# Optimization experiments

Hardware: AMD Instinct MI355X
Metric: run time of the kernel (lower is better)

## Reference

```python
import jax, jax.numpy as jnp
import numpy as np
import math

B = 64
N = 2048
EMBED_DIM = 128
N_HEADS = 8
VAL_DIM = EMBED_DIM // N_HEADS  # 16
KEY_DIM = VAL_DIM               # key_dim defaults to val_dim
CLIP = True
NORM = 1.0 / math.sqrt(KEY_DIM)


def _uniform_param(k, shape):
    # torch init: uniform(-stdv, stdv) with stdv = 1/sqrt(size(-1))
    stdv = 1.0 / math.sqrt(shape[-1])
    return jax.random.uniform(k, shape, jnp.float32, -stdv, stdv)


def setup_inputs() -> dict:
    key = jax.random.key(0)
    ks = jax.random.split(key, 11)
    h = jax.random.normal(ks[0], (B, N, EMBED_DIM), jnp.float32)
    adj_c = jax.random.randint(ks[1], (B, N, N), 0, 2).astype(jnp.float32)
    phone_set = jax.random.randint(ks[2], (B,), 1, N - 1)
    return dict(
        h=h, adj_c=adj_c, phone_set=phone_set,
        Wq_bf=_uniform_param(ks[3], (EMBED_DIM, KEY_DIM)),
        Wk_bf=_uniform_param(ks[4], (EMBED_DIM, KEY_DIM)),
        Wv_bf=_uniform_param(ks[5], (EMBED_DIM, VAL_DIM)),
        Wo_bf=_uniform_param(ks[6], (VAL_DIM, EMBED_DIM)),
        Wq_af=_uniform_param(ks[7], (EMBED_DIM, KEY_DIM)),
        Wk_af=_uniform_param(ks[8], (EMBED_DIM, KEY_DIM)),
        Wv_af=_uniform_param(ks[9], (EMBED_DIM, VAL_DIM)),
        Wo_af=_uniform_param(ks[10], (VAL_DIM, EMBED_DIM)),
    )


def _attend(h, h_phone, adj_row, pos_mask, Wq, Wk, Wv, Wo):
    # h: (B,N,D), h_phone: (B,D), adj_row: (B,N), pos_mask: (B,N) bool
    Q = h_phone @ Wq                              # (B,K)
    K = jnp.einsum('bnd,dk->bnk', h, Wk)          # (B,N,K)
    V = jnp.einsum('bnd,dk->bnk', h, Wv)          # (B,N,V)
    compat = NORM * jnp.einsum('bk,bnk->bn', Q, K)
    if CLIP:
        compat = 10.0 * jnp.tanh(compat)
    valid = pos_mask & (adj_row != 0)
    # masked stable softmax over valid positions; fully-masked rows -> zeros
    mx = jnp.max(jnp.where(valid, compat, -jnp.inf), axis=-1, keepdims=True)
    mx = jnp.where(jnp.isfinite(mx), mx, 0.0)
    e = jnp.where(valid, jnp.exp(compat - mx), 0.0)
    s = jnp.sum(e, axis=-1, keepdims=True)
    attn = (e / jnp.where(s > 0, s, 1.0)) * adj_row   # matches attn * adj slice
    head = jnp.einsum('bn,bnk->bk', attn, V)          # (B,V)
    return head @ Wo                                  # (B,D)


def reference(h, adj_c, phone_set, Wq_bf, Wk_bf, Wv_bf, Wo_bf,
              Wq_af, Wk_af, Wv_af, Wo_af):
    b, n, d = h.shape
    bidx = jnp.arange(b)
    h_phone = h[bidx, phone_set]        # (B,D) single query per graph
    adj_row = adj_c[bidx, phone_set]    # (B,N) adjacency row of phone node
    pos = jnp.arange(n)[None, :]
    mask_bf = pos < phone_set[:, None]   # indices [0, phone)
    mask_af = pos >= phone_set[:, None]  # indices [phone, N)
    g_bf = _attend(h, h_phone, adj_row, mask_bf, Wq_bf, Wk_bf, Wv_bf, Wo_bf)
    g_af = _attend(h, h_phone, adj_row, mask_af, Wq_af, Wk_af, Wv_af, Wo_af)
    return (g_bf, g_af)
```

## Files before the change

kernel.cpp:

```cpp
#include <hip/hip_runtime.h>
#include <math.h>

#define BB 64
#define NN 2048
#define DD 128
#define KD 16
#define NORMF 0.25f
#define CHUNK 32
#define PSTRIDE 260
#define WS_PART (BB * 2 * DD)

__device__ __forceinline__ void wave_lds_fence() {
    asm volatile("s_waitcnt lgkmcnt(0)" ::: "memory");
    __builtin_amdgcn_wave_barrier();
}

__global__ __launch_bounds__(256)
void setup_w(const float* __restrict__ h, const int* __restrict__ phone,
             const float* __restrict__ Wq_bf, const float* __restrict__ Wk_bf,
             const float* __restrict__ Wq_af, const float* __restrict__ Wk_af,
             float* __restrict__ ws)
{
    const int b = blockIdx.x;
    const int tid = threadIdx.x;
    __shared__ float hp[DD];
    __shared__ float qpart[32][8];
    __shared__ float q[2][KD];

    if (tid < DD) hp[tid] = h[((size_t)b * NN + phone[b]) * DD + tid];
    __syncthreads();

    {
        const int pair = tid >> 3, sub = tid & 7;
        const int br = pair >> 4, k = pair & 15;
        const float* Wq = br ? Wq_af : Wq_bf;
        float acc = 0.f;
        #pragma unroll
        for (int i = 0; i < 16; ++i) {
            const int d = sub * 16 + i;
            acc += hp[d] * Wq[d * KD + k];
        }
        qpart[pair][sub] = acc;
    }
    __syncthreads();
    if (tid < 32) {
        float acc = 0.f;
        #pragma unroll
        for (int i = 0; i < 8; ++i) acc += qpart[tid][i];
        q[tid >> 4][tid & 15] = acc;
    }
    __syncthreads();

    {
        const int br = tid >> 7, d = tid & 127;
        const float* Wk = br ? Wk_af : Wk_bf;
        float acc = 0.f;
        #pragma unroll
        for (int k = 0; k < KD; ++k) acc += Wk[d * KD + k] * q[br][k];
        ws[((size_t)b * 2 + br) * DD + d] = NORMF * acc;
    }
}

template <int P>
__global__ __launch_bounds__(256)
void attn_main(const float* __restrict__ h,
               const float* __restrict__ adj,
               const int*   __restrict__ phone,
               float* __restrict__ ws)
{
    constexpr int K = 16 / P;
    const int tid  = threadIdx.x;
    const int wid  = tid >> 6;
    const int lane = tid & 63;
    const int half = lane >> 5;
    const int l    = lane & 31;
    const int dbase = 4 * l;

    const int xcd  = blockIdx.x & 7;
    const int slot = blockIdx.x >> 3;
    const int b    = xcd + 8 * (slot / P);
    const int bip  = slot % P;
    const int ph   = phone[b];

    __shared__ float part[4][CHUNK][33];
    __shared__ float ea_s[4][CHUNK];
    __shared__ float red_h[4][2][DD];
    __shared__ float red_s[4][2];

    const float* adjrow = adj + ((size_t)b * NN + ph) * NN;
    const float* hb     = h + (size_t)b * NN * DD;
    const int chbase    = (bip * 4 + wid) * K;

    float adjv[K];
    #pragma unroll
    for (int c = 0; c < K; ++c) adjv[c] = adjrow[(chbase + c) * CHUNK + l];

    const float* wp = ws + (size_t)b * 2 * DD;
    const float4 wbf = *(const float4*)(wp + dbase);
    const float4 waf = *(const float4*)(wp + DD + dbase);

    float sbf = 0.f, saf = 0.f;
    float hgbf[4] = {0, 0, 0, 0}, hgaf[4] = {0, 0, 0, 0};

    #pragma unroll
    for (int c = 0; c < K; ++c) {
        const int n0 = (chbase + c) * CHUNK;
        const unsigned long long mask = __ballot(adjv[c] != 0.f);

        float4 hv[16];
        #pragma unroll
        for (int t = 0; t < 16; ++t) {
            const int r = 2 * t + half;
            hv[t] = make_float4(0.f, 0.f, 0.f, 0.f);
            if ((mask >> r) & 1ull)
                hv[t] = *(const float4*)(hb + (size_t)(n0 + r) * DD + dbase);
        }

        #pragma unroll
        for (int t = 0; t < 16; ++t) {
            const int r = 2 * t + half;
            const float4 w = ((n0 + r) >= ph) ? waf : wbf;
            part[wid][r][l] = hv[t].x * w.x + hv[t].y * w.y + hv[t].z * w.z + hv[t].w * w.w;
        }
        wave_lds_fence();

        float a0 = 0.f, a1 = 0.f, a2 = 0.f, a3 = 0.f;
        #pragma unroll
        for (int j = 0; j < 32; j += 4) {
            a0 += part[wid][l][j];
            a1 += part[wid][l][j + 1];
            a2 += part[wid][l][j + 2];
            a3 += part[wid][l][j + 3];
        }
        const float p = (a0 + a1) + (a2 + a3);
        const float e = __expf(10.f * tanhf(p) - 10.f);
        const float es = (adjv[c] != 0.f) ? e : 0.f;
        const float ea = es * adjv[c];
        const bool rowaf = (n0 + l) >= ph;
        sbf += rowaf ? 0.f : es;
        saf += rowaf ? es : 0.f;
        if (lane < 32) ea_s[wid][l] = ea;
        wave_lds_fence();

        #pragma unroll
        for (int t = 0; t < 16; ++t) {
            const int r = 2 * t + half;
            const float ear = ea_s[wid][r];
            const bool af = (n0 + r) >= ph;
            const float eb = af ? 0.f : ear;
            const float ef = af ? ear : 0.f;
            hgbf[0] += eb * hv[t].x; hgbf[1] += eb * hv[t].y;
            hgbf[2] += eb * hv[t].z; hgbf[3] += eb * hv[t].w;
            hgaf[0] += ef * hv[t].x; hgaf[1] += ef * hv[t].y;
            hgaf[2] += ef * hv[t].z; hgaf[3] += ef * hv[t].w;
        }
    }

    #pragma unroll
    for (int m = 1; m <= 16; m <<= 1) {
        sbf += __shfl_xor(sbf, m, 64);
        saf += __shfl_xor(saf, m, 64);
    }
    #pragma unroll
    for (int i = 0; i < 4; ++i) {
        hgbf[i] += __shfl_xor(hgbf[i], 32, 64);
        hgaf[i] += __shfl_xor(hgaf[i], 32, 64);
    }
    if (lane < 32) {
        #pragma unroll
        for (int i = 0; i < 4; ++i) {
            red_h[wid][0][dbase + i] = hgbf[i];
            red_h[wid][1][dbase + i] = hgaf[i];
        }
    }
    if (lane == 0) { red_s[wid][0] = sbf; red_s[wid][1] = saf; }
    __syncthreads();

    {
        const int br = tid >> 7, d = tid & 127;
        float* op = ws + WS_PART + (size_t)(b * P + bip) * PSTRIDE;
        op[br * DD + d] = red_h[0][br][d] + red_h[1][br][d] + red_h[2][br][d] + red_h[3][br][d];
        if (tid < 2)
            op[2 * DD + tid] = red_s[0][tid] + red_s[1][tid] + red_s[2][tid] + red_s[3][tid];
    }
}

template <int P>
__global__ __launch_bounds__(256)
void finalize_kernel(const float* __restrict__ Wv_bf, const float* __restrict__ Wo_bf,
                     const float* __restrict__ Wv_af, const float* __restrict__ Wo_af,
                     const float* __restrict__ ws, float* __restrict__ out)
{
    const int b = blockIdx.x;
    const int tid = threadIdx.x;
    __shared__ float hs[2][DD];
    __shared__ float ssum[2];
    __shared__ float hpart[32][8];
    __shared__ float head[2][KD];

    const float* base = ws + WS_PART + (size_t)b * P * PSTRIDE;
    {
        const int br = tid >> 7, d = tid & 127;
        float acc = 0.f;
        #pragma unroll
        for (int p = 0; p < P; ++p) acc += base[(size_t)p * PSTRIDE + br * DD + d];
        hs[br][d] = acc;
    }
    if (tid < 2) {
        float acc = 0.f;
        #pragma unroll
        for (int p = 0; p < P; ++p) acc += base[(size_t)p * PSTRIDE + 2 * DD + tid];
        ssum[tid] = acc;
    }
    __syncthreads();

    {
        const int pair = tid >> 3, sub = tid & 7;
        const int br = pair >> 4, k = pair & 15;
        const float* Wv = br ? Wv_af : Wv_bf;
        float acc = 0.f;
        #pragma unroll
        for (int i = 0; i < 16; ++i) {
            const int d = sub * 16 + i;
            acc += hs[br][d] * Wv[d * KD + k];
        }
        hpart[pair][sub] = acc;
    }
    __syncthreads();
    if (tid < 32) {
        float acc = 0.f;
        #pragma unroll
        for (int i = 0; i < 8; ++i) acc += hpart[tid][i];
        head[tid >> 4][tid & 15] = acc;
    }
    __syncthreads();

    {
        const int br = tid >> 7, j = tid & 127;
        const float s = ssum[br];
        const float inv = (s > 0.f) ? 1.f / s : 0.f;
        const float* Wo = br ? Wo_af : Wo_bf;
        float acc = 0.f;
        #pragma unroll
        for (int k = 0; k < KD; ++k) acc += head[br][k] * Wo[k * DD + j];
        out[br * BB * DD + b * DD + j] = acc * inv;
    }
}

extern "C" void kernel_launch(void* const* d_in, const int* in_sizes, int n_in,
                              void* d_out, int out_size, void* d_ws, size_t ws_size,
                              hipStream_t stream) {
    const float* h     = (const float*)d_in[0];
    const float* adj   = (const float*)d_in[1];
    const int*   phone = (const int*)d_in[2];
    const float* Wq_bf = (const float*)d_in[3];
    const float* Wk_bf = (const float*)d_in[4];
    const float* Wv_bf = (const float*)d_in[5];
    const float* Wo_bf = (const float*)d_in[6];
    const float* Wq_af = (const float*)d_in[7];
    const float* Wk_af = (const float*)d_in[8];
    const float* Wv_af = (const float*)d_in[9];
    const float* Wo_af = (const float*)d_in[10];

    float* out = (float*)d_out;
    float* ws  = (float*)d_ws;

    int P = 16;
    while (P > 1 && (size_t)(WS_PART + (size_t)BB * P * PSTRIDE) * sizeof(float) > ws_size)
        P >>= 1;

    setup_w<<<BB, 256, 0, stream>>>(h, phone, Wq_bf, Wk_bf, Wq_af, Wk_af, ws);

    switch (P) {
    case 16:
        attn_main<16><<<BB * 16, 256, 0, stream>>>(h, adj, phone, ws);
        finalize_kernel<16><<<BB, 256, 0, stream>>>(Wv_bf, Wo_bf, Wv_af, Wo_af, ws, out);
        break;
    case 8:
        attn_main<8><<<BB * 8, 256, 0, stream>>>(h, adj, phone, ws);
        finalize_kernel<8><<<BB, 256, 0, stream>>>(Wv_bf, Wo_bf, Wv_af, Wo_af, ws, out);
        break;
    case 4:
        attn_main<4><<<BB * 4, 256, 0, stream>>>(h, adj, phone, ws);
        finalize_kernel<4><<<BB, 256, 0, stream>>>(Wv_bf, Wo_bf, Wv_af, Wo_af, ws, out);
        break;
    case 2:
        attn_main<2><<<BB * 2, 256, 0, stream>>>(h, adj, phone, ws);
        finalize_kernel<2><<<BB, 256, 0, stream>>>(Wv_bf, Wo_bf, Wv_af, Wo_af, ws, out);
        break;
    default:
        attn_main<1><<<BB, 256, 0, stream>>>(h, adj, phone, ws);
        finalize_kernel<1><<<BB, 256, 0, stream>>>(Wv_bf, Wo_bf, Wv_af, Wo_af, ws, out);
        break;
    }
}
```

Before: 20.49 us.

## Fuse query/key-weight setup into attention kernel and prefetch finalize weights

Removes the separate setup kernel by having every attention block recompute the phone query projection and the Wk·q vector into shared memory, saving one kernel launch and the global round trip through the workspace. Each of the 1024 blocks now repeats the small 128x16 matvecs and adds three block barriers before the main loop. The finalize kernel also loads its Wv and Wo weights into registers before waiting on the partial-sum reduction, so those global loads can overlap.

Measured after the change: 19.17 us. -6.5%, faster.

```diff
diff --git a/kernel.cpp b/kernel.cpp
--- a/kernel.cpp
+++ b/kernel.cpp
@@ -8,57 +8,10 @@
 #define NORMF 0.25f
 #define CHUNK 32
 #define PSTRIDE 260
-#define WS_PART (BB * 2 * DD)
 
 __device__ __forceinline__ void wave_lds_fence() {
     asm volatile("s_waitcnt lgkmcnt(0)" ::: "memory");
     __builtin_amdgcn_wave_barrier();
-}
-
-__global__ __launch_bounds__(256)
-void setup_w(const float* __restrict__ h, const int* __restrict__ phone,
-             const float* __restrict__ Wq_bf, const float* __restrict__ Wk_bf,
-             const float* __restrict__ Wq_af, const float* __restrict__ Wk_af,
-             float* __restrict__ ws)
-{
-    const int b = blockIdx.x;
-    const int tid = threadIdx.x;
-    __shared__ float hp[DD];
-    __shared__ float qpart[32][8];
-    __shared__ float q[2][KD];
-
-    if (tid < DD) hp[tid] = h[((size_t)b * NN + phone[b]) * DD + tid];
-    __syncthreads();
-
-    {
-        const int pair = tid >> 3, sub = tid & 7;
-        const int br = pair >> 4, k = pair & 15;
-        const float* Wq = br ? Wq_af : Wq_bf;
-        float acc = 0.f;
-        #pragma unroll
-        for (int i = 0; i < 16; ++i) {
-            const int d = sub * 16 + i;
-            acc += hp[d] * Wq[d * KD + k];
-        }
-        qpart[pair][sub] = acc;
-    }
-    __syncthreads();
-    if (tid < 32) {
-        float acc = 0.f;
-        #pragma unroll
-        for (int i = 0; i < 8; ++i) acc += qpart[tid][i];
-        q[tid >> 4][tid & 15] = acc;
-    }
-    __syncthreads();
-
-    {
-        const int br = tid >> 7, d = tid & 127;
-        const float* Wk = br ? Wk_af : Wk_bf;
-        float acc = 0.f;
-        #pragma unroll
-        for (int k = 0; k < KD; ++k) acc += Wk[d * KD + k] * q[br][k];
-        ws[((size_t)b * 2 + br) * DD + d] = NORMF * acc;
-    }
 }
 
 template <int P>
@@ -66,6 +19,8 @@
 void attn_main(const float* __restrict__ h,
                const float* __restrict__ adj,
                const int*   __restrict__ phone,
+               const float* __restrict__ Wq_bf, const float* __restrict__ Wk_bf,
+               const float* __restrict__ Wq_af, const float* __restrict__ Wk_af,
                float* __restrict__ ws)
 {
     constexpr int K = 16 / P;
@@ -82,22 +37,58 @@
     const int bip  = slot % P;
     const int ph   = phone[b];
 
+    __shared__ float hp[DD];
+    __shared__ float qpart[32][8];
+    __shared__ float q[2][KD];
+    __shared__ float w_s[2][DD];
     __shared__ float part[4][CHUNK][33];
     __shared__ float ea_s[4][CHUNK];
     __shared__ float red_h[4][2][DD];
     __shared__ float red_s[4][2];
 
+    const float* hb     = h + (size_t)b * NN * DD;
     const float* adjrow = adj + ((size_t)b * NN + ph) * NN;
-    const float* hb     = h + (size_t)b * NN * DD;
     const int chbase    = (bip * 4 + wid) * K;
 
     float adjv[K];
     #pragma unroll
     for (int c = 0; c < K; ++c) adjv[c] = adjrow[(chbase + c) * CHUNK + l];
 
-    const float* wp = ws + (size_t)b * 2 * DD;
-    const float4 wbf = *(const float4*)(wp + dbase);
-    const float4 waf = *(const float4*)(wp + DD + dbase);
+    if (tid < DD) hp[tid] = hb[(size_t)ph * DD + tid];
+    __syncthreads();
+
+    {
+        const int pair = tid >> 3, sub = tid & 7;
+        const int br = pair >> 4, k = pair & 15;
+        const float* Wq = br ? Wq_af : Wq_bf;
+        float acc = 0.f;
+        #pragma unroll
+        for (int i = 0; i < 16; ++i) {
+            const int d = sub * 16 + i;
+            acc += hp[d] * Wq[d * KD + k];
+        }
+        qpart[pair][sub] = acc;
+    }
+    __syncthreads();
+    if (tid < 32) {
+        float acc = 0.f;
+        #pragma unroll
+        for (int i = 0; i < 8; ++i) acc += qpart[tid][i];
+        q[tid >> 4][tid & 15] = acc;
+    }
+    __syncthreads();
+    {
+        const int br = tid >> 7, d = tid & 127;
+        const float* Wk = br ? Wk_af : Wk_bf;
+        float acc = 0.f;
+        #pragma unroll
+        for (int k = 0; k < KD; ++k) acc += Wk[d * KD + k] * q[br][k];
+        w_s[br][d] = NORMF * acc;
+    }
+    __syncthreads();
+
+    const float4 wbf = *(const float4*)(&w_s[0][dbase]);
+    const float4 waf = *(const float4*)(&w_s[1][dbase]);
 
     float sbf = 0.f, saf = 0.f;
     float hgbf[4] = {0, 0, 0, 0}, hgaf[4] = {0, 0, 0, 0};
@@ -178,7 +169,7 @@
 
     {
         const int br = tid >> 7, d = tid & 127;
-        float* op = ws + WS_PART + (size_t)(b * P + bip) * PSTRIDE;
+        float* op = ws + (size_t)(b * P + bip) * PSTRIDE;
         op[br * DD + d] = red_h[0][br][d] + red_h[1][br][d] + red_h[2][br][d] + red_h[3][br][d];
         if (tid < 2)
             op[2 * DD + tid] = red_s[0][tid] + red_s[1][tid] + red_s[2][tid] + red_s[3][tid];
@@ -198,13 +189,25 @@
     __shared__ float hpart[32][8];
     __shared__ float head[2][KD];
 
-    const float* base = ws + WS_PART + (size_t)b * P * PSTRIDE;
-    {
-        const int br = tid >> 7, d = tid & 127;
-        float acc = 0.f;
-        #pragma unroll
-        for (int p = 0; p < P; ++p) acc += base[(size_t)p * PSTRIDE + br * DD + d];
-        hs[br][d] = acc;
+    const int pair = tid >> 3, sub = tid & 7;
+    const int brv = pair >> 4, kv = pair & 15;
+    const float* Wv = brv ? Wv_af : Wv_bf;
+    float wvr[16];
+    #pragma unroll
+    for (int i = 0; i < 16; ++i) wvr[i] = Wv[(sub * 16 + i) * KD + kv];
+
+    const int br2 = tid >> 7, j = tid & 127;
+    const float* Wo = br2 ? Wo_af : Wo_bf;
+    float wor[KD];
+    #pragma unroll
+    for (int k = 0; k < KD; ++k) wor[k] = Wo[k * DD + j];
+
+    const float* base = ws + (size_t)b * P * PSTRIDE;
+    {
+        float acc = 0.f;
+        #pragma unroll
+        for (int p = 0; p < P; ++p) acc += base[(size_t)p * PSTRIDE + br2 * DD + j];
+        hs[br2][j] = acc;
     }
     if (tid < 2) {
         float acc = 0.f;
@@ -215,15 +218,9 @@
     __syncthreads();
 
     {
-        const int pair = tid >> 3, sub = tid & 7;
-        const int br = pair >> 4, k = pair & 15;
-        const float* Wv = br ? Wv_af : Wv_bf;
-        float acc = 0.f;
-        #pragma unroll
-        for (int i = 0; i < 16; ++i) {
-            const int d = sub * 16 + i;
-            acc += hs[br][d] * Wv[d * KD + k];
-        }
+        float acc = 0.f;
+        #pragma unroll
+        for (int i = 0; i < 16; ++i) acc += hs[brv][sub * 16 + i] * wvr[i];
         hpart[pair][sub] = acc;
     }
     __syncthreads();
@@ -236,14 +233,12 @@
     __syncthreads();
 
     {
-        const int br = tid >> 7, j = tid & 127;
-        const float s = ssum[br];
+        const float s = ssum[br2];
         const float inv = (s > 0.f) ? 1.f / s : 0.f;
-        const float* Wo = br ? Wo_af : Wo_bf;
-        float acc = 0.f;
-        #pragma unroll
-        for (int k = 0; k < KD; ++k) acc += head[br][k] * Wo[k * DD + j];
-        out[br * BB * DD + b * DD + j] = acc * inv;
+        float acc = 0.f;
+        #pragma unroll
+        for (int k = 0; k < KD; ++k) acc += head[br2][k] * wor[k];
+        out[br2 * BB * DD + b * DD + j] = acc * inv;
     }
 }
 
@@ -266,30 +261,27 @@
     float* ws  = (float*)d_ws;
 
     int P = 16;
-    while (P > 1 && (size_t)(WS_PART + (size_t)BB * P * PSTRIDE) * sizeof(float) > ws_size)
-        P >>= 1;
-
-    setup_w<<<BB, 256, 0, stream>>>(h, phone, Wq_bf, Wk_bf, Wq_af, Wk_af, ws);
+    while (P > 1 && (size_t)BB * P * PSTRIDE * sizeof(float) > ws_size) P >>= 1;
 
     switch (P) {
     case 16:
-        attn_main<16><<<BB * 16, 256, 0, stream>>>(h, adj, phone, ws);
+        attn_main<16><<<BB * 16, 256, 0, stream>>>(h, adj, phone, Wq_bf, Wk_bf, Wq_af, Wk_af, ws);
         finalize_kernel<16><<<BB, 256, 0, stream>>>(Wv_bf, Wo_bf, Wv_af, Wo_af, ws, out);
         break;
     case 8:
-        attn_main<8><<<BB * 8, 256, 0, stream>>>(h, adj, phone, ws);
+        attn_main<8><<<BB * 8, 256, 0, stream>>>(h, adj, phone, Wq_bf, Wk_bf, Wq_af, Wk_af, ws);
         finalize_kernel<8><<<BB, 256, 0, stream>>>(Wv_bf, Wo_bf, Wv_af, Wo_af, ws, out);
         break;
     case 4:
-        attn_main<4><<<BB * 4, 256, 0, stream>>>(h, adj, phone, ws);
+        attn_main<4><<<BB * 4, 256, 0, stream>>>(h, adj, phone, Wq_bf, Wk_bf, Wq_af, Wk_af, ws);
         finalize_kernel<4><<<BB, 256, 0, stream>>>(Wv_bf, Wo_bf, Wv_af, Wo_af, ws, out);
         break;
     case 2:
-        attn_main<2><<<BB * 2, 256, 0, stream>>>(h, adj, phone, ws);
+        attn_main<2><<<BB * 2, 256, 0, stream>>>(h, adj, phone, Wq_bf, Wk_bf, Wq_af, Wk_af, ws);
         finalize_kernel<2><<<BB, 256, 0, stream>>>(Wv_bf, Wo_bf, Wv_af, Wo_af, ws, out);
         break;
     default:
-        attn_main<1><<<BB, 256, 0, stream>>>(h, adj, phone, ws);
+        attn_main<1><<<BB, 256, 0, stream>>>(h, adj, phone, Wq_bf, Wk_bf, Wq_af, Wk_af, ws);
         finalize_kernel<1><<<BB, 256, 0, stream>>>(Wv_bf, Wo_bf, Wv_af, Wo_af, ws, out);
         break;
     }
```
